# Kernel tuning notes

Hardware: AMD Instinct MI355X
Metric: run time of the kernel (lower is better)

The kernel has to match this reference:

```python
import jax, jax.numpy as jnp
import numpy as np

D_MODEL = 2048
NUM_HEADS = 16
HEAD_DIM = 128
BATCH = 4
SEQ = 2048


def setup_inputs() -> dict:
    key = jax.random.key(0)
    ks = jax.random.split(key, 5)
    s = 0.02
    return {
        "x": jax.random.normal(ks[0], (BATCH, SEQ, D_MODEL), dtype=jnp.float32),
        "Wq": jax.random.normal(ks[1], (NUM_HEADS * HEAD_DIM, D_MODEL), dtype=jnp.float32) * s,
        "Wk": jax.random.normal(ks[2], (NUM_HEADS * HEAD_DIM, D_MODEL), dtype=jnp.float32) * s,
        "Wv": jax.random.normal(ks[3], (NUM_HEADS * HEAD_DIM, D_MODEL), dtype=jnp.float32) * s,
        "Wo": jax.random.normal(ks[4], (D_MODEL, NUM_HEADS * HEAD_DIM), dtype=jnp.float32) * s,
    }


def _split_heads(t):
    b, s, _ = t.shape
    return t.reshape(b, s, NUM_HEADS, HEAD_DIM).transpose(0, 2, 1, 3)  # [b,h,s,d]


def reference(x, Wq, Wk, Wv, Wo):
    # prefill: QKV proj + causal SDPA + output proj. torch Linear: x @ W.T
    q = _split_heads(x @ Wq.T)
    k = _split_heads(x @ Wk.T)
    v = _split_heads(x @ Wv.T)
    scale = 1.0 / jnp.sqrt(jnp.asarray(HEAD_DIM, dtype=x.dtype))
    scores = jnp.einsum("bhqd,bhkd->bhqk", q, k) * scale
    causal = jnp.tril(jnp.ones((SEQ, SEQ), dtype=bool))
    scores = jnp.where(causal, scores, jnp.finfo(scores.dtype).min)
    attn = jax.nn.softmax(scores, axis=-1)
    y = jnp.einsum("bhqk,bhkd->bhqd", attn, v)
    y = y.transpose(0, 2, 1, 3).reshape(x.shape[0], SEQ, NUM_HEADS * HEAD_DIM)
    y = y @ Wo.T
    return (y, k, v)
```

## Files before the change

kernel.cpp:

```cpp
#include <hip/hip_runtime.h>
#include <stdint.h>

#define DM 2048
#define NH 16
#define HD 128
#define BB 4
#define SS 2048
#define BS (BB*SS)
#define NQKV (3*DM)
#define SCQ 0.12751744565f

typedef __bf16 bf16_t;
typedef __attribute__((ext_vector_type(8))) __bf16 bf16x8;
typedef __attribute__((ext_vector_type(4))) float f32x4;
typedef __attribute__((ext_vector_type(16))) float f32x16;
typedef __attribute__((ext_vector_type(4))) float float4v;
typedef __attribute__((ext_vector_type(4))) unsigned int uint4v;
typedef __attribute__((ext_vector_type(4))) unsigned short ushort4v;
typedef __attribute__((ext_vector_type(8))) unsigned short ushort8;

__device__ __forceinline__ unsigned short f2bf(float f) {
  unsigned u = __float_as_uint(f);
  u += 0x7fffu + ((u >> 16) & 1u);
  return (unsigned short)(u >> 16);
}

__device__ __forceinline__ void gl16(const void* g, void* l) {
  __builtin_amdgcn_global_load_lds(
      (const __attribute__((address_space(1))) unsigned int*)(unsigned long long)g,
      (__attribute__((address_space(3))) unsigned int*)(unsigned int)(unsigned long long)l,
      16, 0, 0);
}

__global__ void conv_all(const float* __restrict__ x,  const float* __restrict__ wq,
                         const float* __restrict__ wk, const float* __restrict__ wv,
                         const float* __restrict__ wo,
                         unsigned short* __restrict__ xbf,
                         unsigned short* __restrict__ wqkv,
                         unsigned short* __restrict__ wobf) {
  const int NX = BS * DM / 4;
  const int NW = DM * DM / 4;
  int i = blockIdx.x * blockDim.x + threadIdx.x;
  int stride = gridDim.x * blockDim.x;
  for (; i < NX + 4 * NW; i += stride) {
    const float4v* src;
    ushort4v* dst;
    if (i < NX)               { src = (const float4v*)x  + i;            dst = (ushort4v*)xbf + i; }
    else if (i < NX + NW)     { int j = i - NX;          src = (const float4v*)wq + j; dst = (ushort4v*)wqkv + j; }
    else if (i < NX + 2 * NW) { int j = i - NX - NW;     src = (const float4v*)wk + j; dst = (ushort4v*)wqkv + NW + j; }
    else if (i < NX + 3 * NW) { int j = i - NX - 2 * NW; src = (const float4v*)wv + j; dst = (ushort4v*)wqkv + 2 * NW + j; }
    else                      { int j = i - NX - 3 * NW; src = (const float4v*)wo + j; dst = (ushort4v*)wobf + j; }
    float4v v = *src;
    ushort4v o;
    o.x = f2bf(v.x); o.y = f2bf(v.y); o.z = f2bf(v.z); o.w = f2bf(v.w);
    *dst = o;
  }
}

__global__ void vtrans(const float* __restrict__ vf, bf16_t* __restrict__ vt) {
  __shared__ unsigned short T[128 * 64];
  const int t = threadIdx.x;
  const int s0 = blockIdx.x * 64;
  const int bh = blockIdx.y;
  const size_t in_off = (size_t)bh * SS * HD;
  const int sr = t >> 5, c4 = t & 31;
#pragma unroll
  for (int j = 0; j < 8; ++j) {
    int s = j * 8 + sr;
    float4v v = *(const float4v*)(vf + in_off + (size_t)(s0 + s) * HD + c4 * 4);
#pragma unroll
    for (int q = 0; q < 4; ++q) {
      int d = c4 * 4 + q;
      int bc = s * 2;
      int byt = d * 128 + ((((bc >> 4) ^ (d & 7)) << 4) | (bc & 15));
      *(unsigned short*)((char*)T + byt) = f2bf(v[q]);
    }
  }
  __syncthreads();
  const int dr = t >> 3, c8 = t & 7;
  unsigned short* out = (unsigned short*)vt + (size_t)bh * HD * SS;
#pragma unroll
  for (int j = 0; j < 4; ++j) {
    int d = j * 32 + dr;
    ushort8 val = *(const ushort8*)((char*)T + d * 128 + ((c8 ^ (d & 7)) << 4));
    *(ushort8*)(out + (size_t)d * SS + s0 + c8 * 8) = val;
  }
}

template<int MODE>
__global__ void gemm64(const bf16_t* __restrict__ A, const bf16_t* __restrict__ Bm,
                       const int K, const int N,
                       float* __restrict__ Cf,
                       bf16_t* __restrict__ qbf, bf16_t* __restrict__ kbt,
                       float* __restrict__ kf, float* __restrict__ vf) {
  __shared__ bf16_t As[2][128 * 64];
  __shared__ bf16_t Bs[2][128 * 64];
  const int t = threadIdx.x;
  const int w = t >> 6, lane = t & 63;
  const int wm = (w >> 1) * 64, wn = (w & 1) * 64;
  const int row0 = blockIdx.x * 128, col0 = blockIdx.y * 128;
  const int fr = lane & 15, fq = lane >> 4;
  const int NT = K >> 6;

  const bf16_t* Asrc[4];
  const bf16_t* Bsrc[4];
  int dst[4];
#pragma unroll
  for (int j = 0; j < 4; ++j) {
    int u = j * 256 + t, r = u >> 3, c = u & 7;
    Asrc[j] = A + (size_t)(row0 + r) * K + ((c ^ ((r >> 1) & 7)) * 8);
    Bsrc[j] = Bm + (size_t)(col0 + r) * K + ((c ^ ((r >> 1) & 7)) * 8);
    dst[j] = u * 16;
  }

  f32x4 acc[4][4] = {};

#pragma unroll
  for (int j = 0; j < 4; ++j) {
    gl16(Asrc[j], (char*)(&As[0][0]) + dst[j]);
    gl16(Bsrc[j], (char*)(&Bs[0][0]) + dst[j]);
  }

  for (int T = 0; T < NT; ++T) {
    const int cur = T & 1;
    __syncthreads();

    if (T + 1 < NT) {
      const size_t ko = (size_t)(T + 1) * 64;
#pragma unroll
      for (int j = 0; j < 4; ++j) {
        gl16(Asrc[j] + ko, (char*)(&As[cur ^ 1][0]) + dst[j]);
        gl16(Bsrc[j] + ko, (char*)(&Bs[cur ^ 1][0]) + dst[j]);
      }
    }

    const bf16_t* al = &As[cur][0];
    const bf16_t* bl = &Bs[cur][0];
#pragma unroll
    for (int ks = 0; ks < 2; ++ks) {
      bf16x8 af[4], bfv[4];
#pragma unroll
      for (int f = 0; f < 4; ++f) {
        int ra = wm + f * 16 + fr;
        af[f] = *(const bf16x8*)(al + ra * 64 + (((fq + ks * 4) ^ ((ra >> 1) & 7)) * 8));
        int rb = wn + f * 16 + fr;
        bfv[f] = *(const bf16x8*)(bl + rb * 64 + (((fq + ks * 4) ^ ((rb >> 1) & 7)) * 8));
      }
#pragma unroll
      for (int i = 0; i < 4; ++i)
#pragma unroll
        for (int jn = 0; jn < 4; ++jn)
          acc[i][jn] = __builtin_amdgcn_mfma_f32_16x16x32_bf16(af[i], bfv[jn], acc[i][jn], 0, 0, 0);
    }
  }

#pragma unroll
  for (int i = 0; i < 4; ++i) {
#pragma unroll
    for (int jn = 0; jn < 4; ++jn) {
#pragma unroll
      for (int r = 0; r < 4; ++r) {
        int m = row0 + wm + i * 16 + fq * 4 + r;
        int n = col0 + wn + jn * 16 + fr;
        float v = acc[i][jn][r];
        if (MODE == 0) {
          Cf[(size_t)m * N + n] = v;
        } else {
          int b = m >> 11, s = m & 2047;
          if (n < DM) {
            int h = n >> 7, d = n & 127;
            qbf[(((size_t)(b * NH + h)) * SS + s) * HD + d] = (bf16_t)(v * SCQ);
          } else if (n < 2 * DM) {
            int nn = n - DM, h = nn >> 7, d = nn & 127;
            size_t o = (((size_t)(b * NH + h)) * SS + s) * HD + d;
            kbt[o] = (bf16_t)v;
            kf[o] = v;
          } else {
            int nn = n - 2 * DM, h = nn >> 7, d = nn & 127;
            vf[(((size_t)(b * NH + h)) * SS + s) * HD + d] = v;
          }
        }
      }
    }
  }
}

__global__ __launch_bounds__(256, 2)
void attn_fwd5(const bf16_t* __restrict__ qbf, const bf16_t* __restrict__ kbf,
               const bf16_t* __restrict__ vt, bf16_t* __restrict__ aout) {
  __shared__ bf16_t Ks[2][64 * 128];
  __shared__ bf16_t Vs[2][64 * 128];
  const int t = threadIdx.x, w = t >> 6, lane = t & 63;
  const int l31 = lane & 31, hi = lane >> 5;
  const int orig = blockIdx.x;
  const int wg = (orig & 7) * 128 + (orig >> 3);
  const int bh = wg >> 4;
  const int qt = 15 - (wg & 15);
  const int q0 = qt * 128;
  const int nt = 2 * qt + 2;
  const size_t bh_off = (size_t)bh * SS * HD;
  const char* kbase = (const char*)(kbf + bh_off);
  const char* vbase = (const char*)(vt + bh_off);

  const char* ksrc[4];
  const char* vsrc[4];
#pragma unroll
  for (int i = 0; i < 4; ++i) {
    int r = (w * 4 + i) * 4 + (lane >> 4);
    int c = (lane & 15) ^ (r & 15);
    ksrc[i] = kbase + r * 256 + c * 16;
    int d = 2 * r + (c >> 3);
    vsrc[i] = vbase + (size_t)d * (SS * 2) + (c & 7) * 16;
  }

  bf16x8 qfr[8];
  {
    const char* qrow = (const char*)(qbf + bh_off + (size_t)(q0 + w * 32 + l31) * HD);
#pragma unroll
    for (int ds = 0; ds < 8; ++ds)
      qfr[ds] = *(const bf16x8*)(qrow + ds * 32 + hi * 16);
  }

#pragma unroll
  for (int i = 0; i < 4; ++i) {
    gl16(ksrc[i], (char*)(&Ks[0][0]) + (w * 4 + i) * 1024);
    gl16(vsrc[i], (char*)(&Vs[0][0]) + (w * 4 + i) * 1024);
    ksrc[i] += 16384;
    vsrc[i] += 128;
  }

  float mrow = -3.0e38f, lrow = 0.f;
  f32x16 accO[4] = {};

  auto make_pa = [&](const f32x16& sv, bf16x8& paA, bf16x8& paB) {
    unsigned W[8];
#pragma unroll
    for (int m = 0; m < 8; ++m) {
      float lo = sv[2 * m], hh = sv[2 * m + 1];
      asm("v_cvt_pk_bf16_f32 %0, %1, %2" : "=v"(W[m]) : "v"(lo), "v"(hh));
    }
    asm volatile("v_permlane32_swap_b32 %0, %1" : "+v"(W[0]), "+v"(W[2]));
    asm volatile("v_permlane32_swap_b32 %0, %1" : "+v"(W[1]), "+v"(W[3]));
    asm volatile("v_permlane32_swap_b32 %0, %1" : "+v"(W[4]), "+v"(W[6]));
    asm volatile("v_permlane32_swap_b32 %0, %1" : "+v"(W[5]), "+v"(W[7]));
    uint4v u0; u0.x = W[0]; u0.y = W[1]; u0.z = W[2]; u0.w = W[3];
    paA = __builtin_bit_cast(bf16x8, u0);
    uint4v u1; u1.x = W[4]; u1.y = W[5]; u1.z = W[6]; u1.w = W[7];
    paB = __builtin_bit_cast(bf16x8, u1);
  };

  for (int kt = 0; kt < nt; ++kt) {
    const int cur = kt & 1;
    __syncthreads();

    if (kt + 1 < nt) {
#pragma unroll
      for (int i = 0; i < 4; ++i) {
        gl16(ksrc[i], (char*)(&Ks[cur ^ 1][0]) + (w * 4 + i) * 1024);
        gl16(vsrc[i], (char*)(&Vs[cur ^ 1][0]) + (w * 4 + i) * 1024);
        ksrc[i] += 16384;
        vsrc[i] += 128;
      }
    }

    const char* kl = (const char*)&Ks[cur][0];
    f32x16 s0 = {}, s1 = {};
    const int rck = l31 & 15;
    __builtin_amdgcn_s_setprio(1);
#pragma unroll
    for (int ds = 0; ds < 8; ++ds) {
      int ch = ((2 * ds + hi) ^ rck) << 4;
      bf16x8 kf0 = *(const bf16x8*)(kl + l31 * 256 + ch);
      s0 = __builtin_amdgcn_mfma_f32_32x32x16_bf16(kf0, qfr[ds], s0, 0, 0, 0);
      bf16x8 kf1 = *(const bf16x8*)(kl + (32 + l31) * 256 + ch);
      s1 = __builtin_amdgcn_mfma_f32_32x32x16_bf16(kf1, qfr[ds], s1, 0, 0, 0);
    }
    __builtin_amdgcn_s_setprio(0);

    const int kv0 = kt * 64;
    if (kt >= 2 * qt) {
      const int qg = q0 + w * 32 + l31;
#pragma unroll
      for (int r = 0; r < 16; ++r) {
        int klo = kv0 + (r & 3) + 8 * (r >> 2) + 4 * hi;
        if (klo > qg) s0[r] = -3.0e38f;
        if (klo + 32 > qg) s1[r] = -3.0e38f;
      }
    }
    float rm = s0[0];
#pragma unroll
    for (int r = 1; r < 16; ++r) rm = fmaxf(rm, s0[r]);
#pragma unroll
    for (int r = 0; r < 16; ++r) rm = fmaxf(rm, s1[r]);
    rm = fmaxf(rm, __shfl_xor(rm, 32, 64));
    if (__ballot(rm > mrow + 8.0f)) {
      float mnew = fmaxf(mrow, rm);
      float fct = __builtin_amdgcn_exp2f(mrow - mnew);
      mrow = mnew;
      lrow *= fct;
#pragma unroll
      for (int r = 0; r < 16; ++r) {
        float f = __shfl(fct, (r & 3) + 8 * (r >> 2) + 4 * hi, 64);
        accO[0][r] *= f; accO[1][r] *= f; accO[2][r] *= f; accO[3][r] *= f;
      }
    }
    float ss = 0.f;
#pragma unroll
    for (int r = 0; r < 16; ++r) { float p = __builtin_amdgcn_exp2f(s0[r] - mrow); s0[r] = p; ss += p; }
#pragma unroll
    for (int r = 0; r < 16; ++r) { float p = __builtin_amdgcn_exp2f(s1[r] - mrow); s1[r] = p; ss += p; }
    ss += __shfl_xor(ss, 32, 64);
    lrow += ss;

    bf16x8 pa00, pa01, pa10, pa11;
    make_pa(s0, pa00, pa01);
    make_pa(s1, pa10, pa11);

    const char* vl = (const char*)&Vs[cur][0];
    __builtin_amdgcn_s_setprio(1);
#pragma unroll
    for (int dt = 0; dt < 4; ++dt) {
      int R = dt * 16 + (l31 >> 1);
      int cb = (l31 & 1) << 3;
      int rx = R & 15;
      bf16x8 v00 = *(const bf16x8*)(vl + R * 256 + (((cb + 0 + hi) ^ rx) << 4));
      accO[dt] = __builtin_amdgcn_mfma_f32_32x32x16_bf16(pa00, v00, accO[dt], 0, 0, 0);
      bf16x8 v01 = *(const bf16x8*)(vl + R * 256 + (((cb + 2 + hi) ^ rx) << 4));
      accO[dt] = __builtin_amdgcn_mfma_f32_32x32x16_bf16(pa01, v01, accO[dt], 0, 0, 0);
      bf16x8 v10 = *(const bf16x8*)(vl + R * 256 + (((cb + 4 + hi) ^ rx) << 4));
      accO[dt] = __builtin_amdgcn_mfma_f32_32x32x16_bf16(pa10, v10, accO[dt], 0, 0, 0);
      bf16x8 v11 = *(const bf16x8*)(vl + R * 256 + (((cb + 6 + hi) ^ rx) << 4));
      accO[dt] = __builtin_amdgcn_mfma_f32_32x32x16_bf16(pa11, v11, accO[dt], 0, 0, 0);
    }
    __builtin_amdgcn_s_setprio(0);
  }

  const int b = bh >> 4, h = bh & 15;
#pragma unroll
  for (int r = 0; r < 16; ++r) {
    int qr = (r & 3) + 8 * (r >> 2) + 4 * hi;
    float inv = __builtin_amdgcn_rcpf(__shfl(lrow, qr, 64));
    int srow = q0 + w * 32 + qr;
    bf16_t* orow = aout + ((size_t)(b * SS + srow)) * DM + h * HD + l31;
    orow[0]  = (bf16_t)(accO[0][r] * inv);
    orow[32] = (bf16_t)(accO[1][r] * inv);
    orow[64] = (bf16_t)(accO[2][r] * inv);
    orow[96] = (bf16_t)(accO[3][r] * inv);
  }
}

extern "C" void kernel_launch(void* const* d_in, const int* in_sizes, int n_in,
                              void* d_out, int out_size, void* d_ws, size_t ws_size,
                              hipStream_t stream) {
  (void)in_sizes; (void)n_in; (void)out_size; (void)ws_size;
  const float* x  = (const float*)d_in[0];
  const float* Wq = (const float*)d_in[1];
  const float* Wk = (const float*)d_in[2];
  const float* Wv = (const float*)d_in[3];
  const float* Wo = (const float*)d_in[4];

  float* y  = (float*)d_out;
  float* kf = y + (size_t)BS * DM;
  float* vf = kf + (size_t)BS * DM;

  char* ws = (char*)d_ws;
  bf16_t* xbf  = (bf16_t*)ws;
  bf16_t* abf  = xbf;
  bf16_t* qbf  = (bf16_t*)(ws + (size_t)32 * 1024 * 1024);
  bf16_t* wqkv = (bf16_t*)(ws + (size_t)64 * 1024 * 1024);
  bf16_t* wobf = (bf16_t*)(ws + (size_t)88 * 1024 * 1024);
  bf16_t* kbt  = (bf16_t*)y;
  bf16_t* vtb  = (bf16_t*)((char*)y + (size_t)32 * 1024 * 1024);

  conv_all<<<2048, 256, 0, stream>>>(x, Wq, Wk, Wv, Wo,
                                     (unsigned short*)xbf, (unsigned short*)wqkv,
                                     (unsigned short*)wobf);

  gemm64<1><<<dim3(BS / 128, NQKV / 128), 256, 0, stream>>>(
      xbf, wqkv, DM, NQKV, nullptr, qbf, kbt, kf, vf);

  vtrans<<<dim3(SS / 64, BB * NH), 256, 0, stream>>>(vf, vtb);

  attn_fwd5<<<1024, 256, 0, stream>>>(qbf, kbt, vtb, abf);

  gemm64<0><<<dim3(BS / 128, DM / 128), 256, 0, stream>>>(
      abf, wobf, DM, DM, y, nullptr, nullptr, nullptr, nullptr);
}
```

Measured before the change: 446.2 us.

## Replace double-buffered GEMM with four-stage K=32 ring pipeline using vmcnt waits

Rewrites the projection GEMM to use a 4-slot LDS ring of 32-wide K tiles, with three tiles in flight. Explicit s_waitcnt vmcnt counts and a raw s_barrier replace the full __syncthreads. This lets each step wait only for the oldest load. It aims to hide global-load latency better than the two-stage 64-wide scheme, but it halves MFMA work per barrier and relies on the hand-counted vmcnt values being correct.

```diff
diff --git a/kernel.cpp b/kernel.cpp
--- a/kernel.cpp
+++ b/kernel.cpp
@@ -88,71 +88,72 @@
 }
 
 template<int MODE>
-__global__ void gemm64(const bf16_t* __restrict__ A, const bf16_t* __restrict__ Bm,
-                       const int K, const int N,
-                       float* __restrict__ Cf,
-                       bf16_t* __restrict__ qbf, bf16_t* __restrict__ kbt,
-                       float* __restrict__ kf, float* __restrict__ vf) {
-  __shared__ bf16_t As[2][128 * 64];
-  __shared__ bf16_t Bs[2][128 * 64];
+__global__ void gemmr(const bf16_t* __restrict__ A, const bf16_t* __restrict__ Bm,
+                      const int K, const int N,
+                      float* __restrict__ Cf,
+                      bf16_t* __restrict__ qbf, bf16_t* __restrict__ kbt,
+                      float* __restrict__ kf, float* __restrict__ vf) {
+  __shared__ bf16_t As[4][128 * 32];
+  __shared__ bf16_t Bs[4][128 * 32];
   const int t = threadIdx.x;
   const int w = t >> 6, lane = t & 63;
   const int wm = (w >> 1) * 64, wn = (w & 1) * 64;
   const int row0 = blockIdx.x * 128, col0 = blockIdx.y * 128;
   const int fr = lane & 15, fq = lane >> 4;
-  const int NT = K >> 6;
-
-  const bf16_t* Asrc[4];
-  const bf16_t* Bsrc[4];
-  int dst[4];
-#pragma unroll
-  for (int j = 0; j < 4; ++j) {
-    int u = j * 256 + t, r = u >> 3, c = u & 7;
-    Asrc[j] = A + (size_t)(row0 + r) * K + ((c ^ ((r >> 1) & 7)) * 8);
-    Bsrc[j] = Bm + (size_t)(col0 + r) * K + ((c ^ ((r >> 1) & 7)) * 8);
+  const int NT = K >> 5;
+
+  const bf16_t* Asrc[2];
+  const bf16_t* Bsrc[2];
+  int dst[2];
+#pragma unroll
+  for (int j = 0; j < 2; ++j) {
+    int u = j * 256 + t, r = u >> 2, c = u & 3;
+    Asrc[j] = A + (size_t)(row0 + r) * K + ((c ^ ((r >> 1) & 3)) * 8);
+    Bsrc[j] = Bm + (size_t)(col0 + r) * K + ((c ^ ((r >> 1) & 3)) * 8);
     dst[j] = u * 16;
   }
+  const int swz = ((fq ^ ((fr >> 1) & 3)) * 8);
 
   f32x4 acc[4][4] = {};
 
-#pragma unroll
-  for (int j = 0; j < 4; ++j) {
-    gl16(Asrc[j], (char*)(&As[0][0]) + dst[j]);
-    gl16(Bsrc[j], (char*)(&Bs[0][0]) + dst[j]);
-  }
+#define STAGE(TT)                                                   \
+  {                                                                 \
+    const int sl_ = (TT) & 3;                                       \
+    const size_t ko_ = (size_t)(TT) * 32;                           \
+    gl16(Asrc[0] + ko_, (char*)(&As[sl_][0]) + dst[0]);             \
+    gl16(Asrc[1] + ko_, (char*)(&As[sl_][0]) + dst[1]);             \
+    gl16(Bsrc[0] + ko_, (char*)(&Bs[sl_][0]) + dst[0]);             \
+    gl16(Bsrc[1] + ko_, (char*)(&Bs[sl_][0]) + dst[1]);             \
+  }
+
+  STAGE(0); STAGE(1); STAGE(2);
 
   for (int T = 0; T < NT; ++T) {
-    const int cur = T & 1;
-    __syncthreads();
-
-    if (T + 1 < NT) {
-      const size_t ko = (size_t)(T + 1) * 64;
-#pragma unroll
-      for (int j = 0; j < 4; ++j) {
-        gl16(Asrc[j] + ko, (char*)(&As[cur ^ 1][0]) + dst[j]);
-        gl16(Bsrc[j] + ko, (char*)(&Bs[cur ^ 1][0]) + dst[j]);
-      }
-    }
-
-    const bf16_t* al = &As[cur][0];
-    const bf16_t* bl = &Bs[cur][0];
-#pragma unroll
-    for (int ks = 0; ks < 2; ++ks) {
-      bf16x8 af[4], bfv[4];
-#pragma unroll
-      for (int f = 0; f < 4; ++f) {
-        int ra = wm + f * 16 + fr;
-        af[f] = *(const bf16x8*)(al + ra * 64 + (((fq + ks * 4) ^ ((ra >> 1) & 7)) * 8));
-        int rb = wn + f * 16 + fr;
-        bfv[f] = *(const bf16x8*)(bl + rb * 64 + (((fq + ks * 4) ^ ((rb >> 1) & 7)) * 8));
-      }
-#pragma unroll
-      for (int i = 0; i < 4; ++i)
-#pragma unroll
-        for (int jn = 0; jn < 4; ++jn)
-          acc[i][jn] = __builtin_amdgcn_mfma_f32_16x16x32_bf16(af[i], bfv[jn], acc[i][jn], 0, 0, 0);
-    }
-  }
+    if (T + 2 < NT) {
+      asm volatile("s_waitcnt vmcnt(8)" ::: "memory");
+    } else if (T + 1 < NT) {
+      asm volatile("s_waitcnt vmcnt(4)" ::: "memory");
+    } else {
+      asm volatile("s_waitcnt vmcnt(0)" ::: "memory");
+    }
+    asm volatile("s_barrier" ::: "memory");
+    if (T + 3 < NT) STAGE(T + 3);
+
+    const bf16_t* al = &As[T & 3][0];
+    const bf16_t* bl = &Bs[T & 3][0];
+    bf16x8 af[4], bfv[4];
+#pragma unroll
+    for (int f = 0; f < 4; ++f) {
+      af[f]  = *(const bf16x8*)(al + (wm + f * 16 + fr) * 32 + swz);
+      bfv[f] = *(const bf16x8*)(bl + (wn + f * 16 + fr) * 32 + swz);
+    }
+#pragma unroll
+    for (int i = 0; i < 4; ++i)
+#pragma unroll
+      for (int jn = 0; jn < 4; ++jn)
+        acc[i][jn] = __builtin_amdgcn_mfma_f32_16x16x32_bf16(af[i], bfv[jn], acc[i][jn], 0, 0, 0);
+  }
+#undef STAGE
 
 #pragma unroll
   for (int i = 0; i < 4; ++i) {
@@ -376,13 +377,13 @@
                                      (unsigned short*)xbf, (unsigned short*)wqkv,
                                      (unsigned short*)wobf);
 
-  gemm64<1><<<dim3(BS / 128, NQKV / 128), 256, 0, stream>>>(
+  gemmr<1><<<dim3(BS / 128, NQKV / 128), 256, 0, stream>>>(
       xbf, wqkv, DM, NQKV, nullptr, qbf, kbt, kf, vf);
 
   vtrans<<<dim3(SS / 64, BB * NH), 256, 0, stream>>>(vf, vtb);
 
   attn_fwd5<<<1024, 256, 0, stream>>>(qbf, kbt, vtb, abf);
 
-  gemm64<0><<<dim3(BS / 128, DM / 128), 256, 0, stream>>>(
+  gemmr<0><<<dim3(BS / 128, DM / 128), 256, 0, stream>>>(
       abf, wobf, DM, DM, y, nullptr, nullptr, nullptr, nullptr);
 }
```

Result: slower. 487.8 us (+9.3%).
